# Performance work log

Hardware: AMD Instinct MI355X
Metric: run time of the kernel (lower is better)

Reference implementation:

```python
import jax, jax.numpy as jnp
import numpy as np

BS, N, HD = 16, 96, 128      # batch, nodes per graph, hidden_nf
NL, NS = 4, 2                # n_layers, inv_sublayers
ND, HF = 3, 6                # n_dims, node feature dims (in_node_nf - time)
FIN = HF + 1                 # +1 time channel (condition_time=True)
NF = 100.0                   # normalization_factor, aggregation='sum'


def setup_inputs() -> dict:
    key = jax.random.key(0)
    ks = iter(jax.random.split(key, 40))

    def w(shape, scale=None):
        s = scale if scale is not None else 1.0 / np.sqrt(shape[-2])
        return jax.random.normal(next(ks), shape, jnp.float32) * s

    xh = jax.random.normal(next(ks), (BS, N, ND + HF), jnp.float32)
    t = jnp.array([0.5], jnp.float32)
    nm = (jax.random.uniform(next(ks), (BS, N, 1)) < 0.9).astype(jnp.float32)
    em = nm[:, :, None, :] * nm[:, None, :, :]
    em = em * (1.0 - jnp.eye(N, dtype=jnp.float32)[None, :, :, None])
    G = NL * NS
    return dict(
        xh=xh, t=t, node_mask=nm, edge_mask=em,
        W_emb=w((FIN, HD)), b_emb=jnp.zeros((HD,), jnp.float32),
        gWe1=w((G, 2 * HD + 2, HD)), gbe1=jnp.zeros((G, HD), jnp.float32),
        gWe2=w((G, HD, HD)), gbe2=jnp.zeros((G, HD), jnp.float32),
        gWn1=w((G, 2 * HD, HD)), gbn1=jnp.zeros((G, HD), jnp.float32),
        gWn2=w((G, HD, HD)), gbn2=jnp.zeros((G, HD), jnp.float32),
        eWc1=w((NL, 2 * HD + 2, HD)), ebc1=jnp.zeros((NL, HD), jnp.float32),
        eWc2=w((NL, HD, HD)), ebc2=jnp.zeros((NL, HD), jnp.float32),
        eWc3=w((NL, HD, 1), scale=0.001),   # xavier gain 0.001 as in EDM
        W_out=w((HD, FIN)), b_out=jnp.zeros((FIN,), jnp.float32),
    )


def _pair_mlp(h, ea, W1, b1, W2, b2):
    # silu(Linear(cat([h_i, h_j, ea]))) -> silu(Linear) without materializing the concat
    hi = h @ W1[:HD]            # (B,N,H) source part
    hj = h @ W1[HD:2 * HD]      # (B,N,H) target part
    m = jax.nn.silu(hi[:, :, None, :] + hj[:, None, :, :] + ea @ W1[2 * HD:] + b1)
    return jax.nn.silu(m @ W2 + b2)          # (B,N,N,H)


def _egnn(xh, t, node_mask, edge_mask, W_emb, b_emb, gWe1, gbe1, gWe2, gbe2,
          gWn1, gbn1, gWn2, gbn2, eWc1, ebc1, eWc2, ebc2, eWc3, W_out, b_out):
    xh = xh * node_mask                       # mask padded nodes
    x0 = xh[..., :ND]                         # (B,N,3)
    h_time = jnp.broadcast_to(t.reshape(1, 1, 1), (xh.shape[0], xh.shape[1], 1))
    h = jnp.concatenate([xh[..., ND:], h_time], axis=-1)   # (B,N,FIN)
    h = h @ W_emb + b_emb                     # node embedding
    # initial squared distances (EGNN-level edge_attr, in_edge_nf=1)
    d0 = jnp.sum((x0[:, :, None] - x0[:, None, :]) ** 2, -1, keepdims=True)
    x = x0
    for l in range(NL):                       # EquivariantBlocks
        diff = x[:, :, None] - x[:, None, :]  # x_i - x_j, (B,N,N,3)
        radial = jnp.sum(diff ** 2, -1, keepdims=True)
        coord_diff = diff / jnp.sqrt(radial + 1e-8)   # norm_constant=0
        ea = jnp.concatenate([radial, d0], axis=-1)   # (B,N,N,2)
        for s in range(NS):                   # GCL sublayers
            g = l * NS + s
            m = _pair_mlp(h, ea, gWe1[g], gbe1[g], gWe2[g], gbe2[g]) * edge_mask
            agg = jnp.sum(m, axis=2) / NF     # masked scatter-sum over j onto i
            u = jax.nn.silu(h @ gWn1[g, :HD] + agg @ gWn1[g, HD:] + gbn1[g])
            h = (h + (u @ gWn2[g] + gbn2[g])) * node_mask
        # EquivariantUpdate (tanh=False)
        phi = _pair_mlp(h, ea, eWc1[l], ebc1[l], eWc2[l], ebc2[l])
        trans = coord_diff * (phi @ eWc3[l]) * edge_mask    # (B,N,N,3)
        x = (x + jnp.sum(trans, axis=2) / NF) * node_mask
    h = (h @ W_out + b_out) * node_mask       # embedding_out
    vel = (x - x0) * node_mask
    # remove_mean_with_mask
    n_per = jnp.sum(node_mask, axis=1, keepdims=True)
    vel = vel - (jnp.sum(vel, axis=1, keepdims=True) / n_per) * node_mask
    # drop the appended time channel from h (condition_time=True, context=None)
    return jnp.concatenate([vel, h[..., :HF]], axis=-1)    # (B,N,3+HF)


def reference(xh, t, node_mask, edge_mask, W_emb, b_emb, gWe1, gbe1, gWe2, gbe2,
              gWn1, gbn1, gWn2, gbn2, eWc1, ebc1, eWc2, ebc2, eWc3, W_out, b_out):
    return _egnn(xh, t, node_mask, edge_mask, W_emb, b_emb, gWe1, gbe1, gWe2, gbe2,
                 gWn1, gbn1, gWn2, gbn2, eWc1, ebc1, eWc2, ebc2, eWc3, W_out, b_out)
```

## Files before the change

kernel.cpp:

```cpp
#include <hip/hip_runtime.h>
#include <hip/hip_bf16.h>

#define BSZ 16
#define Nn 96
#define HD 128
#define NDIM 3
#define HFEAT 6
#define FINC 7
#define BN (BSZ*Nn)

typedef const float* fp;
typedef __bf16 bf16x8_t __attribute__((ext_vector_type(8)));
typedef float  f32x4_t  __attribute__((ext_vector_type(4)));

__device__ __forceinline__ float silu(float x){
  float e = __expf(-x);
  return x * __builtin_amdgcn_rcpf(1.f + e);
}
__device__ __forceinline__ unsigned short f2b(float x){
  unsigned u = __float_as_uint(x);
  unsigned r = u + 0x7FFF + ((u>>16)&1);
  return (unsigned short)(r>>16);
}
__device__ __forceinline__ unsigned pkf(float a, float b){
  __hip_bfloat162 h2 = __float22bfloat162_rn(make_float2(a,b));
  return *reinterpret_cast<unsigned*>(&h2);
}


__global__ void k_prep(fp gWe1, fp eWc1, fp gWe2, fp eWc2, fp gWn1, fp gWn2,
                       unsigned short* w1b, unsigned short* w2b,
                       unsigned short* wn1b, unsigned short* wn2b){
  int mid = blockIdx.x;
  if (mid < 12){
    const float* src = (mid<8)? gWe1 + (size_t)mid*258*HD : eWc1 + (size_t)(mid-8)*258*HD;
    unsigned short* dst = w1b + (size_t)mid*32768;
    for (int idx = threadIdx.x; idx < 32768; idx += 256){
      int jj = idx&7, l=(idx>>3)&63, kt=(idx>>9)&3, nt=idx>>11;
      int k = kt*32 + (l>>4)*8 + jj, n = nt*16 + (l&15);
      dst[idx] = f2b(src[(size_t)(k + ((n>>7)<<7))*HD + (n&127)]);
    }
  } else if (mid < 24){
    int m2 = mid-12;
    const float* src = (m2<8)? gWe2 + (size_t)m2*HD*HD : eWc2 + (size_t)(m2-8)*HD*HD;
    unsigned short* dst = w2b + (size_t)m2*HD*HD;
    for (int idx = threadIdx.x; idx < HD*HD; idx += 256){
      int jj = idx&7, l=(idx>>3)&63, kt=(idx>>9)&3, nt=idx>>11;
      int k = kt*32 + (l>>4)*8 + jj, n = nt*16 + (l&15);
      dst[idx] = f2b(src[k*HD+n]);
    }
  } else if (mid < 32){
    int g = mid-24;
    const float* src = gWn1 + (size_t)g*256*HD;
    unsigned short* dst = wn1b + (size_t)g*32768;
    for (int idx = threadIdx.x; idx < 32768; idx += 256){
      int jj = idx&7, l=(idx>>3)&63, kt=(idx>>9)&7, nt=idx>>12;
      int k = kt*32 + (l>>4)*8 + jj, n = nt*16 + (l&15);
      dst[idx] = f2b(src[(size_t)k*HD+n]);
    }
  } else {
    int g = mid-32;
    const float* src = gWn2 + (size_t)g*HD*HD;
    unsigned short* dst = wn2b + (size_t)g*HD*HD;
    for (int idx = threadIdx.x; idx < HD*HD; idx += 256){
      int jj = idx&7, l=(idx>>3)&63, kt=(idx>>9)&3, nt=idx>>11;
      int k = kt*32 + (l>>4)*8 + jj, n = nt*16 + (l&15);
      dst[idx] = f2b(src[k*HD+n]);
    }
  }
}

__global__ void k_embed(fp xh, fp t, fp nm, fp W_emb, fp b_emb,
                        float* h, float* x0, float* xA){
  int bn = blockIdx.x, tid = threadIdx.x;
  float nmv = nm[bn];
  if (tid < NDIM){
    float v = xh[bn*(NDIM+HFEAT)+tid] * nmv;
    x0[bn*3+tid] = v; xA[bn*3+tid] = v;
  }
  float acc = b_emb[tid];
  #pragma unroll
  for (int f=0; f<HFEAT; ++f)
    acc += xh[bn*(NDIM+HFEAT)+NDIM+f] * nmv * W_emb[f*HD+tid];
  acc += t[0] * W_emb[HFEAT*HD+tid];
  h[bn*HD+tid] = acc;
}

__global__ __launch_bounds__(256) void k_hij(const float* hin, const unsigned short* w1m,
                                             fp b1, float* Hi, float* Hj){
  __shared__ unsigned int hf[4*256];
  int tid=threadIdx.x, blk=blockIdx.x;
  int b = blk/6, mt = blk%6;
  int l=tid&63, w=tid>>6;
  { int kp=l, jsub=w;
    int kt=kp>>4, q=(kp>>2)&3, dsub=kp&3;
    int sm = kt + 4*(q&1);
    float2 hv[4];
    #pragma unroll
    for(int r=0;r<4;++r)
      hv[r] = ((const float2*)&hin[(size_t)(b*Nn+mt*16+jsub*4+r)*HD])[kp];
    #pragma unroll
    for(int r=0;r<4;++r){
      int row=jsub*4+r;
      hf[kt*256 + (((row + 16*q) ^ sm)<<2) + dsub] = pkf(hv[r].x,hv[r].y);
    } }
  __syncthreads();
  f32x4_t acc[4];
  #pragma unroll
  for(int s=0;s<4;++s) acc[s]=(f32x4_t){0.f,0.f,0.f,0.f};
  #pragma unroll
  for(int kt=0;kt<4;++kt){
    int pl = l ^ (kt + 4*((l>>4)&1));
    bf16x8_t A = *(const bf16x8_t*)((const unsigned int*)hf + kt*256 + pl*4);
    #pragma unroll
    for(int s=0;s<4;++s){
      bf16x8_t B = *(const bf16x8_t*)(w1m + ((((w*4+s)*4+kt)*64 + l)*8));
      acc[s]=__builtin_amdgcn_mfma_f32_16x16x32_bf16(A, B, acc[s], 0,0,0);
    }
  }
  #pragma unroll
  for(int s=0;s<4;++s){
    int nt=w*4+s, n=nt*16+(l&15);
    float b1v = (nt<8)? b1[n] : 0.f;
    #pragma unroll
    for(int r=0;r<4;++r){
      int R = b*Nn + mt*16 + (l>>4)*4 + r;
      float v = acc[s][r];
      if(nt<8) Hi[(size_t)R*HD+n] = v + b1v;
      else     Hj[(size_t)R*HD+(n-128)] = v;
    }
  }
}

__global__ __launch_bounds__(256,4) void k_pair(const float* Hi, const float* Hj,
    const float* x, const float* x0, fp nm, fp W1f,
    const unsigned short* w2m, fp b2, float* agg){
  __shared__ unsigned int m1f[24*256];
  __shared__ float xs[Nn][3], x0s[Nn][3], nms[Nn], rs[Nn], d0s[Nn];
  __shared__ float red[2][HD];
  int tid=threadIdx.x, bn=blockIdx.x;
  int b=bn/Nn, i=bn%Nn;
  int l=tid&63, w=tid>>6, wm=w>>1, wn=w&1;
  int jg=w;

  for(int idx=tid; idx<Nn*3; idx+=256){ int n=idx/3,d=idx%3;
    xs[n][d]=x[(b*Nn+n)*3+d]; x0s[n][d]=x0[(b*Nn+n)*3+d]; }
  if(tid<Nn) nms[tid]=nm[b*Nn+tid];
  __syncthreads();
  if(tid<Nn){
    float dx0=xs[i][0]-xs[tid][0], dx1=xs[i][1]-xs[tid][1], dx2=xs[i][2]-xs[tid][2];
    rs[tid]=dx0*dx0+dx1*dx1+dx2*dx2;
    float e0=x0s[i][0]-x0s[tid][0], e1=x0s[i][1]-x0s[tid][1], e2=x0s[i][2]-x0s[tid][2];
    d0s[tid]=e0*e0+e1*e1+e2*e2;
  }
  __syncthreads();

  { int kp=l;
    int kt2=kp>>4, q=(kp>>2)&3, dsub=kp&3;
    int sm=kt2+4*(q&1);
    float2 hi=((const float2*)&Hi[(size_t)bn*HD])[kp];
    float2 wr=((const float2*)&W1f[(size_t)(2*HD)*HD])[kp];
    float2 wd=((const float2*)&W1f[(size_t)(2*HD+1)*HD])[kp];
    const float2* HjB=(const float2*)&Hj[(size_t)(b*Nn)*HD];
    #pragma unroll
    for(int half=0; half<2; ++half){
      float2 hjv[12];
      #pragma unroll
      for(int u=0;u<12;++u){
        int rr=half*2+(u/6), mt2=u%6;
        int j=mt2*16+jg*4+rr;
        hjv[u]=HjB[(size_t)j*64+kp];
      }
      #pragma unroll
      for(int u=0;u<12;++u){
        int rr=half*2+(u/6), mt2=u%6;
        int jr=jg*4+rr, j=mt2*16+jr;
        float rv=rs[j], dv=d0s[j];
        float m0 =silu(hi.x+hjv[u].x+rv*wr.x+dv*wd.x);
        float m1v=silu(hi.y+hjv[u].y+rv*wr.y+dv*wd.y);
        m1f[mt2*1024 + kt2*256 + (((jr+16*q)^sm)<<2) + dsub]=pkf(m0,m1v);
      }
    } }
  __syncthreads();

  f32x4_t acc[3][4];
  #pragma unroll
  for(int a=0;a<3;++a)
    #pragma unroll
    for(int s=0;s<4;++s) acc[a][s]=(f32x4_t){0.f,0.f,0.f,0.f};
  #pragma unroll
  for(int kt=0;kt<4;++kt){
    int pl = l ^ (kt + 4*((l>>4)&1));
    bf16x8_t Bk[4];
    #pragma unroll
    for(int s=0;s<4;++s)
      Bk[s] = *(const bf16x8_t*)(w2m + ((((wn*4+s)*4+kt)*64 + l)*8));
    #pragma unroll
    for(int a=0;a<3;++a){
      bf16x8_t A = *(const bf16x8_t*)((const unsigned int*)m1f + (((wm*3+a)*4+kt)*256 + pl*4));
      #pragma unroll
      for(int s=0;s<4;++s)
        acc[a][s]=__builtin_amdgcn_mfma_f32_16x16x32_bf16(A, Bk[s], acc[a][s], 0,0,0);
    }
  }

  float b2v[4], p[4]={0.f,0.f,0.f,0.f};
  #pragma unroll
  for(int s=0;s<4;++s) b2v[s]=b2[(wn*4+s)*16 + (l&15)];
  #pragma unroll
  for(int a=0;a<3;++a)
    #pragma unroll
    for(int r=0;r<4;++r){
      int j=(wm*3+a)*16 + (l>>4)*4 + r;
      float emj=(j==i)?0.f:nms[j];
      #pragma unroll
      for(int s=0;s<4;++s) p[s] += silu(acc[a][s][r]+b2v[s])*emj;
    }
  #pragma unroll
  for(int s=0;s<4;++s){ p[s]+=__shfl_xor(p[s],16); p[s]+=__shfl_xor(p[s],32); }
  if(l<16){
    #pragma unroll
    for(int s=0;s<4;++s) red[wm][wn*64 + s*16 + l]=p[s];
  }
  __syncthreads();
  if(tid<HD) agg[(size_t)bn*HD+tid]=(red[0][tid]+red[1][tid])*nms[i]*(1.f/100.f);
}

__global__ __launch_bounds__(256) void k_nodehij(
    const float* hin, float* hout, const float* agg, fp nm,
    const unsigned short* wn1m, fp bn1v, const unsigned short* wn2m, fp bn2v,
    const unsigned short* w1mA, fp b1A, float* HiA, float* HjA,
    const unsigned short* w1mB, fp b1B, float* HiB, float* HjB){
  __shared__ unsigned int af[8*256];
  __shared__ float fbuf[16*132];
  __shared__ float nmr[16];
  int tid=threadIdx.x, blk=blockIdx.x;
  int b=blk/6, mt=blk%6;
  int R0=b*Nn+mt*16;
  int l=tid&63, w=tid>>6;
  int kp=l, jsub=w;
  int kt0=kp>>4, q=(kp>>2)&3, dsub=kp&3;
  int sm=kt0+4*(q&1);
  if(tid<16) nmr[tid]=nm[R0+tid];
  { float2 hv[4], av[4];
    #pragma unroll
    for(int r=0;r<4;++r){
      hv[r]=((const float2*)&hin[(size_t)(R0+jsub*4+r)*HD])[kp];
      av[r]=((const float2*)&agg[(size_t)(R0+jsub*4+r)*HD])[kp];
    }
    #pragma unroll
    for(int r=0;r<4;++r){
      int row=jsub*4+r;
      unsigned off=(((row+16*q)^sm)<<2)+dsub;
      af[kt0*256+off]=pkf(hv[r].x,hv[r].y);
      af[(4+kt0)*256+off]=pkf(av[r].x,av[r].y);
    } }
  __syncthreads();
  f32x4_t c1[2];
  c1[0]=(f32x4_t){0.f,0.f,0.f,0.f}; c1[1]=(f32x4_t){0.f,0.f,0.f,0.f};
  #pragma unroll
  for(int t=0;t<8;++t){
    int pl = l ^ ((t&3) + 4*((l>>4)&1));
    bf16x8_t A=*(const bf16x8_t*)((const unsigned int*)af + t*256 + pl*4);
    #pragma unroll
    for(int s=0;s<2;++s){
      bf16x8_t B=*(const bf16x8_t*)(wn1m + ((((2*w+s)*8+t)*64+l)*8));
      c1[s]=__builtin_amdgcn_mfma_f32_16x16x32_bf16(A,B,c1[s],0,0,0);
    }
  }
  #pragma unroll
  for(int s=0;s<2;++s){
    int n=(2*w+s)*16+(l&15);
    float bv=bn1v[n];
    #pragma unroll
    for(int r=0;r<4;++r){
      int row=(l>>4)*4+r;
      fbuf[row*132+n]=silu(c1[s][r]+bv);
    }
  }
  __syncthreads();
  #pragma unroll
  for(int r=0;r<4;++r){
    int row=jsub*4+r;
    float2 uv=*(const float2*)&fbuf[row*132+2*kp];
    af[kt0*256 + (((row+16*q)^sm)<<2)+dsub]=pkf(uv.x,uv.y);
  }
  __syncthreads();
  f32x4_t c2[2];
  c2[0]=(f32x4_t){0.f,0.f,0.f,0.f}; c2[1]=(f32x4_t){0.f,0.f,0.f,0.f};
  #pragma unroll
  for(int t=0;t<4;++t){
    int pl = l ^ (t + 4*((l>>4)&1));
    bf16x8_t A=*(const bf16x8_t*)((const unsigned int*)af + t*256 + pl*4);
    #pragma unroll
    for(int s=0;s<2;++s){
      bf16x8_t B=*(const bf16x8_t*)(wn2m + ((((2*w+s)*4+t)*64+l)*8));
      c2[s]=__builtin_amdgcn_mfma_f32_16x16x32_bf16(A,B,c2[s],0,0,0);
    }
  }
  { float hv[2][4];
    #pragma unroll
    for(int s=0;s<2;++s){
      int n=(2*w+s)*16+(l&15);
      #pragma unroll
      for(int r=0;r<4;++r)
        hv[s][r]=hin[(size_t)(R0+(l>>4)*4+r)*HD+n];
    }
    #pragma unroll
    for(int s=0;s<2;++s){
      int n=(2*w+s)*16+(l&15);
      float bv=bn2v[n];
      #pragma unroll
      for(int r=0;r<4;++r){
        int row=(l>>4)*4+r;
        float val=(hv[s][r]+c2[s][r]+bv)*nmr[row];
        hout[(size_t)(R0+row)*HD+n]=val;
        fbuf[row*132+n]=val;
      }
    } }
  __syncthreads();
  #pragma unroll
  for(int r=0;r<4;++r){
    int row=jsub*4+r;
    float2 uv=*(const float2*)&fbuf[row*132+2*kp];
    af[kt0*256 + (((row+16*q)^sm)<<2)+dsub]=pkf(uv.x,uv.y);
  }
  __syncthreads();
  {
    f32x4_t a3[4];
    #pragma unroll
    for(int s=0;s<4;++s) a3[s]=(f32x4_t){0.f,0.f,0.f,0.f};
    #pragma unroll
    for(int t=0;t<4;++t){
      int pl = l ^ (t + 4*((l>>4)&1));
      bf16x8_t A=*(const bf16x8_t*)((const unsigned int*)af + t*256 + pl*4);
      #pragma unroll
      for(int s=0;s<4;++s){
        bf16x8_t B=*(const bf16x8_t*)(w1mA + ((((w*4+s)*4+t)*64+l)*8));
        a3[s]=__builtin_amdgcn_mfma_f32_16x16x32_bf16(A,B,a3[s],0,0,0);
      }
    }
    #pragma unroll
    for(int s=0;s<4;++s){
      int nt=w*4+s, n=nt*16+(l&15);
      float b1v=(nt<8)? b1A[n] : 0.f;
      #pragma unroll
      for(int r=0;r<4;++r){
        int R=R0+(l>>4)*4+r;
        float v=a3[s][r];
        if(nt<8) HiA[(size_t)R*HD+n]=v+b1v;
        else     HjA[(size_t)R*HD+(n-128)]=v;
      }
    }
  }
  if(w1mB){
    f32x4_t a3[4];
    #pragma unroll
    for(int s=0;s<4;++s) a3[s]=(f32x4_t){0.f,0.f,0.f,0.f};
    #pragma unroll
    for(int t=0;t<4;++t){
      int pl = l ^ (t + 4*((l>>4)&1));
      bf16x8_t A=*(const bf16x8_t*)((const unsigned int*)af + t*256 + pl*4);
      #pragma unroll
      for(int s=0;s<4;++s){
        bf16x8_t B=*(const bf16x8_t*)(w1mB + ((((w*4+s)*4+t)*64+l)*8));
        a3[s]=__builtin_amdgcn_mfma_f32_16x16x32_bf16(A,B,a3[s],0,0,0);
      }
    }
    #pragma unroll
    for(int s=0;s<4;++s){
      int nt=w*4+s, n=nt*16+(l&15);
      float b1v=(nt<8)? b1B[n] : 0.f;
      #pragma unroll
      for(int r=0;r<4;++r){
        int R=R0+(l>>4)*4+r;
        float v=a3[s][r];
        if(nt<8) HiB[(size_t)R*HD+n]=v+b1v;
        else     HjB[(size_t)R*HD+(n-128)]=v;
      }
    }
  }
}

__global__ __launch_bounds__(256,4) void k_coord(const float* Hi, const float* Hj,
    const float* x, const float* x0, fp nm, fp W1f,
    const unsigned short* w2m, fp b2, fp W3, float* xn){
  __shared__ unsigned int m1f[24*256];
  __shared__ float xs[Nn][3], x0s[Nn][3], nms[Nn], rs[Nn], d0s[Nn];
  __shared__ float redJ[2][Nn];
  __shared__ float sjs[Nn];
  int tid=threadIdx.x, bn=blockIdx.x;
  int b=bn/Nn, i=bn%Nn;
  int l=tid&63, w=tid>>6, wm=w>>1, wn=w&1;
  int jg=w;

  for(int idx=tid; idx<Nn*3; idx+=256){ int n=idx/3,d=idx%3;
    xs[n][d]=x[(b*Nn+n)*3+d]; x0s[n][d]=x0[(b*Nn+n)*3+d]; }
  if(tid<Nn) nms[tid]=nm[b*Nn+tid];
  __syncthreads();
  if(tid<Nn){
    float dx0=xs[i][0]-xs[tid][0], dx1=xs[i][1]-xs[tid][1], dx2=xs[i][2]-xs[tid][2];
    rs[tid]=dx0*dx0+dx1*dx1+dx2*dx2;
    float e0=x0s[i][0]-x0s[tid][0], e1=x0s[i][1]-x0s[tid][1], e2=x0s[i][2]-x0s[tid][2];
    d0s[tid]=e0*e0+e1*e1+e2*e2;
  }
  __syncthreads();

  { int kp=l;
    int kt2=kp>>4, q=(kp>>2)&3, dsub=kp&3;
    int sm=kt2+4*(q&1);
    float2 hi=((const float2*)&Hi[(size_t)bn*HD])[kp];
    float2 wr=((const float2*)&W1f[(size_t)(2*HD)*HD])[kp];
    float2 wd=((const float2*)&W1f[(size_t)(2*HD+1)*HD])[kp];
    const float2* HjB=(const float2*)&Hj[(size_t)(b*Nn)*HD];
    #pragma unroll
    for(int half=0; half<2; ++half){
      float2 hjv[12];
      #pragma unroll
      for(int u=0;u<12;++u){
        int rr=half*2+(u/6), mt2=u%6;
        int j=mt2*16+jg*4+rr;
        hjv[u]=HjB[(size_t)j*64+kp];
      }
      #pragma unroll
      for(int u=0;u<12;++u){
        int rr=half*2+(u/6), mt2=u%6;
        int jr=jg*4+rr, j=mt2*16+jr;
        float rv=rs[j], dv=d0s[j];
        float m0 =silu(hi.x+hjv[u].x+rv*wr.x+dv*wd.x);
        float m1v=silu(hi.y+hjv[u].y+rv*wr.y+dv*wd.y);
        m1f[mt2*1024 + kt2*256 + (((jr+16*q)^sm)<<2) + dsub]=pkf(m0,m1v);
      }
    } }
  __syncthreads();

  f32x4_t acc[3][4];
  #pragma unroll
  for(int a=0;a<3;++a)
    #pragma unroll
    for(int s=0;s<4;++s) acc[a][s]=(f32x4_t){0.f,0.f,0.f,0.f};
  #pragma unroll
  for(int kt=0;kt<4;++kt){
    int pl = l ^ (kt + 4*((l>>4)&1));
    bf16x8_t Bk[4];
    #pragma unroll
    for(int s=0;s<4;++s)
      Bk[s] = *(const bf16x8_t*)(w2m + ((((wn*4+s)*4+kt)*64 + l)*8));
    #pragma unroll
    for(int a=0;a<3;++a){
      bf16x8_t A = *(const bf16x8_t*)((const unsigned int*)m1f + (((wm*3+a)*4+kt)*256 + pl*4));
      #pragma unroll
      for(int s=0;s<4;++s)
        acc[a][s]=__builtin_amdgcn_mfma_f32_16x16x32_bf16(A, Bk[s], acc[a][s], 0,0,0);
    }
  }

  float b2v[4], w3v[4];
  #pragma unroll
  for(int s=0;s<4;++s){ b2v[s]=b2[(wn*4+s)*16+(l&15)]; w3v[s]=W3[(wn*4+s)*16+(l&15)]; }
  float qv[3][4];
  #pragma unroll
  for(int a=0;a<3;++a)
    #pragma unroll
    for(int r=0;r<4;++r){
      float pj=0.f;
      #pragma unroll
      for(int s=0;s<4;++s) pj += silu(acc[a][s][r]+b2v[s])*w3v[s];
      qv[a][r]=pj;
    }
  #pragma unroll
  for(int d=1;d<16;d<<=1)
    #pragma unroll
    for(int a=0;a<3;++a)
      #pragma unroll
      for(int r=0;r<4;++r)
        qv[a][r] += __shfl_xor(qv[a][r], d);
  if((l&15)==0){
    int quad=l>>4;
    #pragma unroll
    for(int a=0;a<3;++a)
      #pragma unroll
      for(int r=0;r<4;++r)
        redJ[wn][(wm*3+a)*16 + quad*4 + r]=qv[a][r];
  }
  __syncthreads();
  if(tid<Nn){
    float pj=redJ[0][tid]+redJ[1][tid];
    float em=(tid==i)?0.f:nms[tid];
    sjs[tid]=pj*em*rsqrtf(rs[tid]+1e-8f);
  }
  __syncthreads();
  if(w<3){
    int d=w;
    float xi=xs[i][d];
    float s=(xi-xs[l][d])*sjs[l];
    if(l<32) s += (xi-xs[l+64][d])*sjs[l+64];
    s+=__shfl_xor(s,1); s+=__shfl_xor(s,2); s+=__shfl_xor(s,4);
    s+=__shfl_xor(s,8); s+=__shfl_xor(s,16); s+=__shfl_xor(s,32);
    if(l==0) xn[(size_t)(b*Nn+i)*3+d]=(xi+s*(1.f/100.f))*nms[i];
  }
}

__global__ void k_velstat(const float* xf, const float* x0, fp nm, float* vstat){
  __shared__ float sh[128];
  int b=blockIdx.x, tid=threadIdx.x;
  float nmv = (tid<Nn)? nm[b*Nn+tid] : 0.f;
  float vals[4];
  #pragma unroll
  for(int d=0;d<3;++d)
    vals[d] = (tid<Nn)? (xf[(b*Nn+tid)*3+d]-x0[(b*Nn+tid)*3+d])*nmv : 0.f;
  vals[3]=nmv;
  #pragma unroll
  for(int q=0;q<4;++q){
    sh[tid]=vals[q]; __syncthreads();
    for(int s=64;s>0;s>>=1){ if(tid<s) sh[tid]+=sh[tid+s]; __syncthreads(); }
    if(tid==0) vstat[b*4+q]=sh[0];
    __syncthreads();
  }
}

__global__ void k_out(const float* h, const float* xf, const float* x0, fp nm,
                      const float* vstat, fp W_out, fp b_out, float* out){
  __shared__ float shh[HD];
  int bn=blockIdx.x, tid=threadIdx.x, b=bn/Nn;
  shh[tid]=h[bn*HD+tid]; __syncthreads();
  float nmv=nm[bn];
  if(tid<3){
    float vel=(xf[bn*3+tid]-x0[bn*3+tid])*nmv;
    float mean=vstat[b*4+tid]/vstat[b*4+3];
    out[bn*(NDIM+HFEAT)+tid]=vel-mean*nmv;
  } else if(tid<3+HFEAT){
    int f=tid-3;
    float acc=b_out[f];
    for(int k=0;k<HD;++k) acc+=shh[k]*W_out[k*FINC+f];
    out[bn*(NDIM+HFEAT)+tid]=acc*nmv;
  }
}

extern "C" void kernel_launch(void* const* d_in, const int* in_sizes, int n_in,
                              void* d_out, int out_size, void* d_ws, size_t ws_size,
                              hipStream_t stream) {
  fp xh   =(fp)d_in[0];
  fp t    =(fp)d_in[1];
  fp nm   =(fp)d_in[2];
  fp W_emb=(fp)d_in[4],  b_emb=(fp)d_in[5];
  fp gWe1 =(fp)d_in[6],  gbe1 =(fp)d_in[7];
  fp gWe2 =(fp)d_in[8],  gbe2 =(fp)d_in[9];
  fp gWn1 =(fp)d_in[10], gbn1 =(fp)d_in[11];
  fp gWn2 =(fp)d_in[12], gbn2 =(fp)d_in[13];
  fp eWc1 =(fp)d_in[14], ebc1 =(fp)d_in[15];
  fp eWc2 =(fp)d_in[16], ebc2 =(fp)d_in[17];
  fp eWc3 =(fp)d_in[18];
  fp W_out=(fp)d_in[19], b_out=(fp)d_in[20];

  unsigned short* w1b  = (unsigned short*)d_ws;
  unsigned short* w2b  = w1b  + (size_t)12*32768;
  unsigned short* wn1b = w2b  + (size_t)12*16384;
  unsigned short* wn2b = wn1b + (size_t)8*32768;
  float* fbase = (float*)(wn2b + (size_t)8*16384);
  float* hA   = fbase;
  float* hB   = hA  + BN*HD;
  float* HiA  = hB  + BN*HD;
  float* HjA  = HiA + BN*HD;
  float* HiE  = HjA + BN*HD;
  float* HjE  = HiE + BN*HD;
  float* agg  = HjE + BN*HD;
  float* x0   = agg + BN*HD;
  float* xA   = x0  + BN*3;
  float* xB   = xA  + BN*3;
  float* vstat= xB  + BN*3;

  k_prep <<<40,256,0,stream>>>(gWe1, eWc1, gWe2, eWc2, gWn1, gWn2, w1b, w2b, wn1b, wn2b);
  k_embed<<<BN,128,0,stream>>>(xh,t,nm,W_emb,b_emb,hA,x0,xA);
  k_hij  <<<96,256,0,stream>>>(hA, w1b, gbe1, HiA, HjA);
  float *hc=hA, *hn=hB, *xc=xA, *xn=xB;
  for(int l=0;l<4;++l){
    int g=2*l;
    k_pair<<<BN,256,0,stream>>>(HiA,HjA,xc,x0,nm, gWe1+(size_t)g*258*HD,
          w2b+(size_t)g*HD*HD, gbe2+(size_t)g*HD, agg);
    k_nodehij<<<96,256,0,stream>>>(hc,hn,agg,nm,
          wn1b+(size_t)g*32768, gbn1+(size_t)g*HD,
          wn2b+(size_t)g*16384, gbn2+(size_t)g*HD,
          w1b+(size_t)(g+1)*32768, gbe1+(size_t)(g+1)*HD, HiA, HjA,
          nullptr, nullptr, nullptr, nullptr);
    { float* tmp=hc; hc=hn; hn=tmp; }
    g=2*l+1;
    k_pair<<<BN,256,0,stream>>>(HiA,HjA,xc,x0,nm, gWe1+(size_t)g*258*HD,
          w2b+(size_t)g*HD*HD, gbe2+(size_t)g*HD, agg);
    bool last = (l==3);
    k_nodehij<<<96,256,0,stream>>>(hc,hn,agg,nm,
          wn1b+(size_t)g*32768, gbn1+(size_t)g*HD,
          wn2b+(size_t)g*16384, gbn2+(size_t)g*HD,
          w1b+(size_t)(8+l)*32768, ebc1+(size_t)l*HD, HiE, HjE,
          last? nullptr : w1b+(size_t)(g+1)*32768,
          last? nullptr : gbe1+(size_t)(g+1)*HD, HiA, HjA);
    { float* tmp=hc; hc=hn; hn=tmp; }
    k_coord<<<BN,256,0,stream>>>(HiE,HjE,xc,x0,nm, eWc1+(size_t)l*258*HD,
          w2b+(size_t)(8+l)*HD*HD, ebc2+(size_t)l*HD,
          eWc3+(size_t)l*HD, xn);
    { float* tmp=xc; xc=xn; xn=tmp; }
  }
  k_velstat<<<BSZ,128,0,stream>>>(xc,x0,nm,vstat);
  k_out   <<<BN,128,0,stream>>>(hc,xc,x0,nm,vstat,W_out,b_out,(float*)d_out);
}
```

Baseline: 430.6 us.

## Split edge-pair kernel over two j-halves and sum partial aggregates downstream

k_pair now launches two blocks per node i, each handling 48 neighbours j with a halved shared-memory tile. Each block writes its partial aggregate to its own buffer, and k_nodehij adds the two halves when it loads them, so no cross-block reduction or atomics are needed. This gives twice as many blocks with less LDS each, aimed at better occupancy and latency hiding. The cost is duplicated loads of Hi, weights and W2 per block and an extra aggregate buffer read. The distance setup in k_pair and k_coord also now reads x and x0 directly from global memory, removing an LDS staging step and a sync.

```diff
diff --git a/kernel.cpp b/kernel.cpp
--- a/kernel.cpp
+++ b/kernel.cpp
@@ -134,24 +134,22 @@
 
 __global__ __launch_bounds__(256,4) void k_pair(const float* Hi, const float* Hj,
     const float* x, const float* x0, fp nm, fp W1f,
-    const unsigned short* w2m, fp b2, float* agg){
-  __shared__ unsigned int m1f[24*256];
-  __shared__ float xs[Nn][3], x0s[Nn][3], nms[Nn], rs[Nn], d0s[Nn];
-  __shared__ float red[2][HD];
-  int tid=threadIdx.x, bn=blockIdx.x;
+    const unsigned short* w2m, fp b2, float* aggH){
+  __shared__ unsigned int m1f[12*256];
+  __shared__ float nms[48], rs[48], d0s[48];
+  int tid=threadIdx.x, blk=blockIdx.x;
+  int bn=blk>>1, half=blk&1;
   int b=bn/Nn, i=bn%Nn;
-  int l=tid&63, w=tid>>6, wm=w>>1, wn=w&1;
-  int jg=w;
-
-  for(int idx=tid; idx<Nn*3; idx+=256){ int n=idx/3,d=idx%3;
-    xs[n][d]=x[(b*Nn+n)*3+d]; x0s[n][d]=x0[(b*Nn+n)*3+d]; }
-  if(tid<Nn) nms[tid]=nm[b*Nn+tid];
-  __syncthreads();
-  if(tid<Nn){
-    float dx0=xs[i][0]-xs[tid][0], dx1=xs[i][1]-xs[tid][1], dx2=xs[i][2]-xs[tid][2];
+  int l=tid&63, w=tid>>6;
+  int jbase=half*48;
+
+  if(tid<48){
+    int jj=b*Nn+jbase+tid, ii=b*Nn+i;
+    float dx0=x[ii*3]-x[jj*3], dx1=x[ii*3+1]-x[jj*3+1], dx2=x[ii*3+2]-x[jj*3+2];
     rs[tid]=dx0*dx0+dx1*dx1+dx2*dx2;
-    float e0=x0s[i][0]-x0s[tid][0], e1=x0s[i][1]-x0s[tid][1], e2=x0s[i][2]-x0s[tid][2];
+    float e0=x0[ii*3]-x0[jj*3], e1=x0[ii*3+1]-x0[jj*3+1], e2=x0[ii*3+2]-x0[jj*3+2];
     d0s[tid]=e0*e0+e1*e1+e2*e2;
+    nms[tid]=nm[jj];
   }
   __syncthreads();
 
@@ -161,73 +159,71 @@
     float2 hi=((const float2*)&Hi[(size_t)bn*HD])[kp];
     float2 wr=((const float2*)&W1f[(size_t)(2*HD)*HD])[kp];
     float2 wd=((const float2*)&W1f[(size_t)(2*HD+1)*HD])[kp];
-    const float2* HjB=(const float2*)&Hj[(size_t)(b*Nn)*HD];
-    #pragma unroll
-    for(int half=0; half<2; ++half){
-      float2 hjv[12];
-      #pragma unroll
-      for(int u=0;u<12;++u){
-        int rr=half*2+(u/6), mt2=u%6;
-        int j=mt2*16+jg*4+rr;
-        hjv[u]=HjB[(size_t)j*64+kp];
-      }
-      #pragma unroll
-      for(int u=0;u<12;++u){
-        int rr=half*2+(u/6), mt2=u%6;
-        int jr=jg*4+rr, j=mt2*16+jr;
-        float rv=rs[j], dv=d0s[j];
-        float m0 =silu(hi.x+hjv[u].x+rv*wr.x+dv*wd.x);
-        float m1v=silu(hi.y+hjv[u].y+rv*wr.y+dv*wd.y);
-        m1f[mt2*1024 + kt2*256 + (((jr+16*q)^sm)<<2) + dsub]=pkf(m0,m1v);
-      }
+    const float2* HjB=(const float2*)&Hj[(size_t)(b*Nn+jbase)*HD];
+    float2 hjv[12];
+    #pragma unroll
+    for(int u=0;u<12;++u){
+      int rr=u>>2, mt2=u&3; if(mt2>2){rr=3; mt2=u-9;}
+      int jl=(u/3)*0; (void)jl;
+      int rr2=u/3, m2=u%3;
+      int jloc=m2*16 + w*4 + rr2;
+      hjv[u]=HjB[(size_t)jloc*64+kp];
+    }
+    #pragma unroll
+    for(int u=0;u<12;++u){
+      int rr2=u/3, m2=u%3;
+      int jr=w*4+rr2, jloc=m2*16+jr;
+      float rv=rs[jloc], dv=d0s[jloc];
+      float m0 =silu(hi.x+hjv[u].x+rv*wr.x+dv*wd.x);
+      float m1v=silu(hi.y+hjv[u].y+rv*wr.y+dv*wd.y);
+      m1f[m2*1024 + kt2*256 + (((jr+16*q)^sm)<<2) + dsub]=pkf(m0,m1v);
     } }
   __syncthreads();
 
-  f32x4_t acc[3][4];
-  #pragma unroll
-  for(int a=0;a<3;++a)
-    #pragma unroll
-    for(int s=0;s<4;++s) acc[a][s]=(f32x4_t){0.f,0.f,0.f,0.f};
+  f32x4_t acc[3][2];
+  #pragma unroll
+  for(int a=0;a<3;++a){ acc[a][0]=(f32x4_t){0.f,0.f,0.f,0.f}; acc[a][1]=(f32x4_t){0.f,0.f,0.f,0.f}; }
   #pragma unroll
   for(int kt=0;kt<4;++kt){
     int pl = l ^ (kt + 4*((l>>4)&1));
-    bf16x8_t Bk[4];
-    #pragma unroll
-    for(int s=0;s<4;++s)
-      Bk[s] = *(const bf16x8_t*)(w2m + ((((wn*4+s)*4+kt)*64 + l)*8));
+    bf16x8_t Bk[2];
+    #pragma unroll
+    for(int s=0;s<2;++s)
+      Bk[s] = *(const bf16x8_t*)(w2m + ((((2*w+s)*4+kt)*64 + l)*8));
     #pragma unroll
     for(int a=0;a<3;++a){
-      bf16x8_t A = *(const bf16x8_t*)((const unsigned int*)m1f + (((wm*3+a)*4+kt)*256 + pl*4));
-      #pragma unroll
-      for(int s=0;s<4;++s)
+      bf16x8_t A = *(const bf16x8_t*)((const unsigned int*)m1f + ((a*4+kt)*256 + pl*4));
+      #pragma unroll
+      for(int s=0;s<2;++s)
         acc[a][s]=__builtin_amdgcn_mfma_f32_16x16x32_bf16(A, Bk[s], acc[a][s], 0,0,0);
     }
   }
 
-  float b2v[4], p[4]={0.f,0.f,0.f,0.f};
-  #pragma unroll
-  for(int s=0;s<4;++s) b2v[s]=b2[(wn*4+s)*16 + (l&15)];
+  float nmi = nm[b*Nn+i];
+  float b2v[2], p[2]={0.f,0.f};
+  #pragma unroll
+  for(int s=0;s<2;++s) b2v[s]=b2[(2*w+s)*16 + (l&15)];
   #pragma unroll
   for(int a=0;a<3;++a)
     #pragma unroll
     for(int r=0;r<4;++r){
-      int j=(wm*3+a)*16 + (l>>4)*4 + r;
-      float emj=(j==i)?0.f:nms[j];
-      #pragma unroll
-      for(int s=0;s<4;++s) p[s] += silu(acc[a][s][r]+b2v[s])*emj;
-    }
-  #pragma unroll
-  for(int s=0;s<4;++s){ p[s]+=__shfl_xor(p[s],16); p[s]+=__shfl_xor(p[s],32); }
+      int jloc=a*16 + (l>>4)*4 + r;
+      int jglob=jbase+jloc;
+      float emj=(jglob==i)?0.f:nms[jloc];
+      #pragma unroll
+      for(int s=0;s<2;++s) p[s] += silu(acc[a][s][r]+b2v[s])*emj;
+    }
+  #pragma unroll
+  for(int s=0;s<2;++s){ p[s]+=__shfl_xor(p[s],16); p[s]+=__shfl_xor(p[s],32); }
   if(l<16){
     #pragma unroll
-    for(int s=0;s<4;++s) red[wm][wn*64 + s*16 + l]=p[s];
-  }
-  __syncthreads();
-  if(tid<HD) agg[(size_t)bn*HD+tid]=(red[0][tid]+red[1][tid])*nms[i]*(1.f/100.f);
+    for(int s=0;s<2;++s)
+      aggH[(size_t)half*BN*HD + (size_t)bn*HD + (2*w+s)*16 + l] = p[s]*nmi*(1.f/100.f);
+  }
 }
 
 __global__ __launch_bounds__(256) void k_nodehij(
-    const float* hin, float* hout, const float* agg, fp nm,
+    const float* hin, float* hout, const float* aggH, fp nm,
     const unsigned short* wn1m, fp bn1v, const unsigned short* wn2m, fp bn2v,
     const unsigned short* w1mA, fp b1A, float* HiA, float* HjA,
     const unsigned short* w1mB, fp b1B, float* HiB, float* HjB){
@@ -242,18 +238,19 @@
   int kt0=kp>>4, q=(kp>>2)&3, dsub=kp&3;
   int sm=kt0+4*(q&1);
   if(tid<16) nmr[tid]=nm[R0+tid];
-  { float2 hv[4], av[4];
+  { float2 hv[4], a0[4], a1[4];
     #pragma unroll
     for(int r=0;r<4;++r){
       hv[r]=((const float2*)&hin[(size_t)(R0+jsub*4+r)*HD])[kp];
-      av[r]=((const float2*)&agg[(size_t)(R0+jsub*4+r)*HD])[kp];
+      a0[r]=((const float2*)&aggH[(size_t)(R0+jsub*4+r)*HD])[kp];
+      a1[r]=((const float2*)&aggH[(size_t)BN*HD+(size_t)(R0+jsub*4+r)*HD])[kp];
     }
     #pragma unroll
     for(int r=0;r<4;++r){
       int row=jsub*4+r;
       unsigned off=(((row+16*q)^sm)<<2)+dsub;
       af[kt0*256+off]=pkf(hv[r].x,hv[r].y);
-      af[(4+kt0)*256+off]=pkf(av[r].x,av[r].y);
+      af[(4+kt0)*256+off]=pkf(a0[r].x+a1[r].x, a0[r].y+a1[r].y);
     } }
   __syncthreads();
   f32x4_t c1[2];
@@ -386,7 +383,7 @@
     const float* x, const float* x0, fp nm, fp W1f,
     const unsigned short* w2m, fp b2, fp W3, float* xn){
   __shared__ unsigned int m1f[24*256];
-  __shared__ float xs[Nn][3], x0s[Nn][3], nms[Nn], rs[Nn], d0s[Nn];
+  __shared__ float xs[Nn][3], nms[Nn], rs[Nn], d0s[Nn];
   __shared__ float redJ[2][Nn];
   __shared__ float sjs[Nn];
   int tid=threadIdx.x, bn=blockIdx.x;
@@ -394,16 +391,16 @@
   int l=tid&63, w=tid>>6, wm=w>>1, wn=w&1;
   int jg=w;
 
+  if(tid<Nn){
+    int jj=b*Nn+tid, ii=b*Nn+i;
+    float dx0=x[ii*3]-x[jj*3], dx1=x[ii*3+1]-x[jj*3+1], dx2=x[ii*3+2]-x[jj*3+2];
+    rs[tid]=dx0*dx0+dx1*dx1+dx2*dx2;
+    float e0=x0[ii*3]-x0[jj*3], e1=x0[ii*3+1]-x0[jj*3+1], e2=x0[ii*3+2]-x0[jj*3+2];
+    d0s[tid]=e0*e0+e1*e1+e2*e2;
+    nms[tid]=nm[jj];
+  }
   for(int idx=tid; idx<Nn*3; idx+=256){ int n=idx/3,d=idx%3;
-    xs[n][d]=x[(b*Nn+n)*3+d]; x0s[n][d]=x0[(b*Nn+n)*3+d]; }
-  if(tid<Nn) nms[tid]=nm[b*Nn+tid];
-  __syncthreads();
-  if(tid<Nn){
-    float dx0=xs[i][0]-xs[tid][0], dx1=xs[i][1]-xs[tid][1], dx2=xs[i][2]-xs[tid][2];
-    rs[tid]=dx0*dx0+dx1*dx1+dx2*dx2;
-    float e0=x0s[i][0]-x0s[tid][0], e1=x0s[i][1]-x0s[tid][1], e2=x0s[i][2]-x0s[tid][2];
-    d0s[tid]=e0*e0+e1*e1+e2*e2;
-  }
+    xs[n][d]=x[(b*Nn+n)*3+d]; }
   __syncthreads();
 
   { int kp=l;
@@ -564,8 +561,8 @@
   float* HjA  = HiA + BN*HD;
   float* HiE  = HjA + BN*HD;
   float* HjE  = HiE + BN*HD;
-  float* agg  = HjE + BN*HD;
-  float* x0   = agg + BN*HD;
+  float* aggH = HjE + BN*HD;
+  float* x0   = aggH+ 2*BN*HD;
   float* xA   = x0  + BN*3;
   float* xB   = xA  + BN*3;
   float* vstat= xB  + BN*3;
@@ -576,19 +573,19 @@
   float *hc=hA, *hn=hB, *xc=xA, *xn=xB;
   for(int l=0;l<4;++l){
     int g=2*l;
-    k_pair<<<BN,256,0,stream>>>(HiA,HjA,xc,x0,nm, gWe1+(size_t)g*258*HD,
-          w2b+(size_t)g*HD*HD, gbe2+(size_t)g*HD, agg);
-    k_nodehij<<<96,256,0,stream>>>(hc,hn,agg,nm,
+    k_pair<<<BN*2,256,0,stream>>>(HiA,HjA,xc,x0,nm, gWe1+(size_t)g*258*HD,
+          w2b+(size_t)g*HD*HD, gbe2+(size_t)g*HD, aggH);
+    k_nodehij<<<96,256,0,stream>>>(hc,hn,aggH,nm,
           wn1b+(size_t)g*32768, gbn1+(size_t)g*HD,
           wn2b+(size_t)g*16384, gbn2+(size_t)g*HD,
           w1b+(size_t)(g+1)*32768, gbe1+(size_t)(g+1)*HD, HiA, HjA,
           nullptr, nullptr, nullptr, nullptr);
     { float* tmp=hc; hc=hn; hn=tmp; }
     g=2*l+1;
-    k_pair<<<BN,256,0,stream>>>(HiA,HjA,xc,x0,nm, gWe1+(size_t)g*258*HD,
-          w2b+(size_t)g*HD*HD, gbe2+(size_t)g*HD, agg);
+    k_pair<<<BN*2,256,0,stream>>>(HiA,HjA,xc,x0,nm, gWe1+(size_t)g*258*HD,
+          w2b+(size_t)g*HD*HD, gbe2+(size_t)g*HD, aggH);
     bool last = (l==3);
-    k_nodehij<<<96,256,0,stream>>>(hc,hn,agg,nm,
+    k_nodehij<<<96,256,0,stream>>>(hc,hn,aggH,nm,
           wn1b+(size_t)g*32768, gbn1+(size_t)g*HD,
           wn2b+(size_t)g*16384, gbn2+(size_t)g*HD,
           w1b+(size_t)(8+l)*32768, ebc1+(size_t)l*HD, HiE, HjE,
```

After: 431.4 us. About the same (+0.2%).
